# Optimization experiments

Hardware: AMD Instinct MI355X
Metric: run time of the kernel (lower is better)

Reference implementation:

```python
import jax, jax.numpy as jnp
import numpy as np

N_NODES = 50000
N_EDGES = 600000
D_IN = 128
HIDDEN = 128
N_REL = 8
N_LAYERS = 2


def setup_inputs() -> dict:
    key = jax.random.key(0)
    ks = jax.random.split(key, 10)
    node_feat = jax.random.normal(ks[0], (N_NODES, D_IN), dtype=jnp.float32)
    edge_index = jax.random.randint(ks[1], (2, N_EDGES), 0, N_NODES, dtype=jnp.int64)
    edge_type = jax.random.randint(ks[2], (N_EDGES,), 0, N_REL, dtype=jnp.int64)
    s = 1.0 / np.sqrt(D_IN)
    # stacked per-layer FastRGCNConv params (input_dim == hidden so shapes match)
    rel_w = jax.random.normal(ks[3], (N_LAYERS, N_REL, D_IN, HIDDEN), dtype=jnp.float32) * s
    root_w = jax.random.normal(ks[4], (N_LAYERS, D_IN, HIDDEN), dtype=jnp.float32) * s
    bias = jax.random.normal(ks[5], (N_LAYERS, HIDDEN), dtype=jnp.float32) * 0.01
    proj_w = jax.random.normal(ks[6], (N_LAYERS * HIDDEN, HIDDEN), dtype=jnp.float32) / np.sqrt(N_LAYERS * HIDDEN)
    proj_b = jax.random.normal(ks[7], (HIDDEN,), dtype=jnp.float32) * 0.01
    return {
        "node_feat": node_feat,
        "edge_index": edge_index,
        "edge_type": edge_type,
        "rel_w": rel_w,
        "root_w": root_w,
        "bias": bias,
        "proj_w": proj_w,
        "proj_b": proj_b,
    }


def _rgcn_layer(x, src, dst, etype, W, root, b):
    # FastRGCNConv: transform all nodes by all relations, then gather per edge.
    xW = jnp.einsum('nd,rdh->nrh', x, W)          # [N, R, H]
    m = xW[src, etype]                             # [E, H] per-edge message
    # mean aggregation per (target, relation), as in PyG FastRGCNConv aggr='mean'
    seg = dst * N_REL + etype                      # combined (target, relation) id
    cnt = jax.ops.segment_sum(jnp.ones_like(etype, dtype=x.dtype), seg,
                              num_segments=N_NODES * N_REL)
    norm = (1.0 / jnp.clip(cnt, 1.0, None))[seg]   # [E]
    agg = jax.ops.segment_sum(m * norm[:, None], dst, num_segments=N_NODES)
    return agg + x @ root + b


def reference(node_feat, edge_index, edge_type, rel_w, root_w, bias, proj_w, proj_b):
    src, dst = edge_index[0], edge_index[1]
    reps = []
    h = node_feat
    for i in range(N_LAYERS):
        h = _rgcn_layer(h, src, dst, edge_type, rel_w[i], root_w[i], bias[i])
        h = jax.nn.relu(h)
        reps.append(h)
    final = jnp.concatenate(reps, axis=-1) @ proj_w + proj_b
    return (final,) + tuple(reps)
```

## Files before the change

kernel.cpp:

```cpp
#include <hip/hip_runtime.h>
#include <hip/hip_bf16.h>

#define NN 50000
#define NE 600000
#define DD 128
#define RR 8
#define KY 1152

#define N2 (NN * RR)
#define SCHUNK 1024
#define NBS2 ((N2 + SCHUNK - 1) / SCHUNK)
#define MGRID ((NN + 127) / 128)

typedef __attribute__((ext_vector_type(8))) short short8;
typedef __attribute__((ext_vector_type(4))) float f32x4;
typedef __attribute__((ext_vector_type(4))) unsigned uint4v;

__device__ __forceinline__ unsigned short f2b(float x){
  __hip_bfloat16 h = __float2bfloat16(x);
  return __builtin_bit_cast(unsigned short, h);
}
__device__ __forceinline__ float blo(unsigned u){ return __builtin_bit_cast(float, u << 16); }
__device__ __forceinline__ float bhi(unsigned u){ return __builtin_bit_cast(float, u & 0xFFFF0000u); }
__device__ __forceinline__ unsigned pack2(float a, float b){
  return (unsigned)f2b(a) | ((unsigned)f2b(b) << 16);
}

#define GLDS16(g, l) __builtin_amdgcn_global_load_lds( \
    (const __attribute__((address_space(1))) void*)(g), \
    (__attribute__((address_space(3))) void*)(l), 16, 0, 0)

__global__ __launch_bounds__(256) void k_hist(const int* __restrict__ ei,
                                              const int* __restrict__ et,
                                              int* __restrict__ cnt) {
  int e = blockIdx.x * 256 + threadIdx.x;
  if (e < NE) {
    int dst = ei[NE + e];
    int r = et[e];
    atomicAdd(&cnt[dst * RR + r], 1);
  }
}

__global__ __launch_bounds__(256) void k_scan1(const int* __restrict__ cnt,
                                               int* __restrict__ bsum) {
  int b = blockIdx.x, t = threadIdx.x;
  int base = b * SCHUNK + t * 4;
  int s = 0;
  if (base < N2) {
    int4 v = *(const int4*)&cnt[base];
    s = v.x + v.y + v.z + v.w;
  }
  #pragma unroll
  for (int off = 32; off; off >>= 1) s += __shfl_down(s, off);
  __shared__ int wsum[4];
  int lane = t & 63, wv = t >> 6;
  if (lane == 0) wsum[wv] = s;
  __syncthreads();
  if (t == 0) bsum[b] = wsum[0] + wsum[1] + wsum[2] + wsum[3];
}

__global__ __launch_bounds__(512) void k_scan2(const int* __restrict__ bsum,
                                               int* __restrict__ boff) {
  int t = threadIdx.x, lane = t & 63, wv = t >> 6;
  int v = (t < NBS2) ? bsum[t] : 0;
  int x = v;
  #pragma unroll
  for (int off = 1; off < 64; off <<= 1) {
    int y = __shfl_up(x, off);
    if (lane >= off) x += y;
  }
  __shared__ int wt[8];
  if (lane == 63) wt[wv] = x;
  __syncthreads();
  int woff = 0;
  for (int w = 0; w < wv; w++) woff += wt[w];
  if (t < NBS2) boff[t] = woff + x - v;
}

__global__ __launch_bounds__(256) void k_scan3(const int* __restrict__ cnt,
                                               const int* __restrict__ boff,
                                               int* __restrict__ rp2,
                                               int* __restrict__ cur2) {
  int b = blockIdx.x, t = threadIdx.x;
  int lane = t & 63, wv = t >> 6;
  int base = b * SCHUNK + t * 4;
  int v[4] = {0, 0, 0, 0};
  int s = 0;
  if (base < N2) {
    int4 q = *(const int4*)&cnt[base];
    v[0] = q.x; v[1] = q.y; v[2] = q.z; v[3] = q.w;
    s = q.x + q.y + q.z + q.w;
  }
  int x = s;
  #pragma unroll
  for (int off = 1; off < 64; off <<= 1) {
    int y = __shfl_up(x, off);
    if (lane >= off) x += y;
  }
  __shared__ int wtot[4];
  if (lane == 63) wtot[wv] = x;
  __syncthreads();
  int woff = 0;
  for (int w = 0; w < wv; w++) woff += wtot[w];
  int exc = boff[b] + woff + x - s;
  if (base < N2) {
    #pragma unroll
    for (int j = 0; j < 4; j++) {
      cur2[base + j] = exc;
      rp2[base + j + 1] = exc + v[j];
      exc += v[j];
    }
  }
  if (b == 0 && t == 0) rp2[0] = 0;
}

__global__ __launch_bounds__(256) void k_scatter(const int* __restrict__ ei,
                                                 const int* __restrict__ et,
                                                 int* __restrict__ cur2,
                                                 unsigned* __restrict__ packed) {
  int e = blockIdx.x * 256 + threadIdx.x;
  if (e < NE) {
    int src = ei[e];
    int dst = ei[NE + e];
    int r = et[e];
    int p = atomicAdd(&cur2[dst * RR + r], 1);
    packed[p] = (unsigned)src | ((unsigned)r << 16);
  }
}

__global__ __launch_bounds__(256) void k_xb(const float* __restrict__ x,
                                            unsigned* __restrict__ xb2) {
  int i = blockIdx.x * 256 + threadIdx.x;
  if (i < NN * (DD / 2)) {
    float2 v = ((const float2*)x)[i];
    xb2[i] = pack2(v.x, v.y);
  }
}

__global__ __launch_bounds__(256) void k_wt2(const float* __restrict__ rel_w,
                                             const float* __restrict__ root_w,
                                             unsigned short* __restrict__ WT2) {
  int idx = blockIdx.x * 256 + threadIdx.x;
  if (idx >= 2 * KY * DD) return;
  int k = idx % DD;
  int j = (idx / DD) % KY;
  int l = idx / (DD * KY);
  float v;
  if (j < RR * DD) v = rel_w[(((size_t)l * RR + (j >> 7)) * DD + k) * DD + (j & 127)];
  else             v = root_w[((size_t)l * DD + k) * DD + (j - RR * DD)];
  WT2[idx] = f2b(v);
}

__global__ __launch_bounds__(256) void k_pt(const float* __restrict__ proj_w,
                                            unsigned short* __restrict__ PT) {
  int idx = blockIdx.x * 256 + threadIdx.x;
  if (idx >= DD * 256) return;
  int k = idx % 256;
  int n = idx / 256;
  PT[idx] = f2b(proj_w[(size_t)k * DD + n]);
}

__global__ __launch_bounds__(256) void k_ygemm(const unsigned short* __restrict__ A, int lda,
                                               const unsigned short* __restrict__ B2,
                                               unsigned short* __restrict__ Y) {
  __shared__ unsigned short smA[128 * 128];
  __shared__ unsigned short smB[128 * 128];
  int t = threadIdx.x;
  int rt = blockIdx.x % MGRID;
  int ct = blockIdx.x / MGRID;
  int lane = t & 63, wv = t >> 6;
  int wm = wv >> 1, wn = wv & 1;
  int l15 = lane & 15, lk = lane >> 4;

  #pragma unroll
  for (int i = 0; i < 8; i++) {
    int f = i * 256 + t;
    int row = f >> 4, cl = f & 15;
    int cg = cl ^ (row & 15);
    int rg = rt * 128 + row; if (rg >= NN) rg = NN - 1;
    GLDS16(A + (size_t)rg * lda + cg * 8, &smA[f * 8]);
  }
  #pragma unroll
  for (int i = 0; i < 8; i++) {
    int f = i * 256 + t;
    int row = f >> 4, cl = f & 15;
    int cg = cl ^ (row & 15);
    GLDS16(B2 + (size_t)(ct * 128 + row) * DD + cg * 8, &smB[f * 8]);
  }
  __syncthreads();

  f32x4 acc[4][4];
  #pragma unroll
  for (int mi = 0; mi < 4; mi++)
    #pragma unroll
    for (int ni = 0; ni < 4; ni++)
      acc[mi][ni] = (f32x4){0.f, 0.f, 0.f, 0.f};

  #pragma unroll
  for (int kk = 0; kk < 4; kk++) {
    short8 af[4], bf[4];
    #pragma unroll
    for (int q = 0; q < 4; q++) {
      int r  = wm * 64 + q * 16 + l15;
      int rb = wn * 64 + q * 16 + l15;
      int c  = kk * 4 + lk;
      af[q] = *(const short8*)&smA[r * 128 + ((c ^ (r & 15)) << 3)];
      bf[q] = *(const short8*)&smB[rb * 128 + ((c ^ (rb & 15)) << 3)];
    }
    #pragma unroll
    for (int mi = 0; mi < 4; mi++)
      #pragma unroll
      for (int ni = 0; ni < 4; ni++)
        acc[mi][ni] = __builtin_amdgcn_mfma_f32_16x16x32_bf16(af[mi], bf[ni], acc[mi][ni], 0, 0, 0);
  }
  __syncthreads();

  #pragma unroll
  for (int mi = 0; mi < 4; mi++)
    #pragma unroll
    for (int ni = 0; ni < 4; ni++) {
      int col = wn * 64 + ni * 16 + l15;
      #pragma unroll
      for (int j = 0; j < 4; j++) {
        int row = wm * 64 + mi * 16 + lk * 4 + j;
        smB[row * 128 + ((((col >> 3) ^ (row & 7)) << 3) | (col & 7))] = f2b(acc[mi][ni][j]);
      }
    }
  __syncthreads();

  {
    int row = t >> 1, half = t & 1;
    int rg = rt * 128 + row;
    if (rg < NN) {
      unsigned short* dst = Y + (size_t)rg * KY + ct * 128 + half * 64;
      #pragma unroll
      for (int i = 0; i < 8; i++) {
        int cc = half * 8 + i;
        ((uint4v*)dst)[i] = *(const uint4v*)&smB[row * 128 + ((cc ^ (row & 7)) << 3)];
      }
    }
  }
}

__global__ __launch_bounds__(256) void k_aggD(const unsigned short* __restrict__ Y,
                                              const unsigned* __restrict__ packed,
                                              const int* __restrict__ rp2,
                                              const float* __restrict__ bias,
                                              float* __restrict__ outf,
                                              unsigned short* __restrict__ hb, int hboff) {
  int v = blockIdx.x * 4 + (threadIdx.x >> 6);
  int lane = threadIdx.x & 63;
  int q = lane >> 4, sub = lane & 15;

  int f = 0;
  if (lane <= 8) f = rp2[v * RR + lane];
  int fn = __shfl(f, lane + 1);
  int c = fn - f;
  float winv = (lane < 8 && c > 0) ? 1.f / (float)c : 0.f;
  int e0 = __shfl(f, 0), e1 = __shfl(f, 8);

  float acc[8];
  #pragma unroll
  for (int j = 0; j < 8; j++) acc[j] = 0.f;

  for (int e = e0 + q; e < e1; e += 4) {
    unsigned rec = packed[e];
    int src = rec & 0xFFFF;
    int r = rec >> 16;
    float w = __shfl(winv, r);
    const uint4v* p = (const uint4v*)(Y + (size_t)src * KY + r * DD + sub * 8);
    uint4v u = *p;
    #pragma unroll
    for (int i = 0; i < 4; i++) {
      acc[2 * i]     += w * blo(u[i]);
      acc[2 * i + 1] += w * bhi(u[i]);
    }
  }

  if (q == 0) {
    uint4v u = *(const uint4v*)(Y + (size_t)v * KY + RR * DD + sub * 8);
    #pragma unroll
    for (int i = 0; i < 4; i++) {
      acc[2 * i]     += blo(u[i]);
      acc[2 * i + 1] += bhi(u[i]);
    }
  }

  #pragma unroll
  for (int j = 0; j < 8; j++) {
    acc[j] += __shfl_xor(acc[j], 32);
    acc[j] += __shfl_xor(acc[j], 16);
  }

  if (q == 0) {
    float4 b0 = *(const float4*)&bias[sub * 8];
    float4 b1 = *(const float4*)&bias[sub * 8 + 4];
    float val[8];
    val[0] = fmaxf(acc[0] + b0.x, 0.f); val[1] = fmaxf(acc[1] + b0.y, 0.f);
    val[2] = fmaxf(acc[2] + b0.z, 0.f); val[3] = fmaxf(acc[3] + b0.w, 0.f);
    val[4] = fmaxf(acc[4] + b1.x, 0.f); val[5] = fmaxf(acc[5] + b1.y, 0.f);
    val[6] = fmaxf(acc[6] + b1.z, 0.f); val[7] = fmaxf(acc[7] + b1.w, 0.f);
    float4* of = (float4*)&outf[(size_t)v * DD + sub * 8];
    of[0] = (float4){val[0], val[1], val[2], val[3]};
    of[1] = (float4){val[4], val[5], val[6], val[7]};
    uint4v hv;
    #pragma unroll
    for (int i = 0; i < 4; i++) hv[i] = pack2(val[2 * i], val[2 * i + 1]);
    *(uint4v*)(hb + (size_t)v * 256 + hboff + sub * 8) = hv;
  }
}

__global__ __launch_bounds__(256) void k_gemm(const unsigned short* __restrict__ A, int lda,
                                              const unsigned short* __restrict__ BT, int ldb,
                                              int M, int K,
                                              const float* __restrict__ bias,
                                              float* __restrict__ outf) {
  __shared__ unsigned short sA[128 * 64];
  __shared__ unsigned short sB[128 * 64];
  int t = threadIdx.x;
  int bm = blockIdx.x;
  int lane = t & 63, wv = t >> 6;
  int wm = wv >> 1, wn = wv & 1;
  int l15 = lane & 15, lk = lane >> 4;

  f32x4 acc[4][4];
  #pragma unroll
  for (int mi = 0; mi < 4; mi++)
    #pragma unroll
    for (int ni = 0; ni < 4; ni++)
      acc[mi][ni] = (f32x4){0.f, 0.f, 0.f, 0.f};

  int nkt = K >> 6;
  for (int kt = 0; kt < nkt; kt++) {
    #pragma unroll
    for (int i = 0; i < 4; i++) {
      int f = i * 256 + t;
      int row = f >> 3, cl = f & 7;
      int cg = cl ^ (row & 7);
      int rg = bm * 128 + row;
      if (rg >= M) rg = M - 1;
      GLDS16(A + (size_t)rg * lda + kt * 64 + cg * 8, &sA[f * 8]);
    }
    #pragma unroll
    for (int i = 0; i < 4; i++) {
      int f = i * 256 + t;
      int row = f >> 3, cl = f & 7;
      int cg = cl ^ (row & 7);
      GLDS16(BT + (size_t)row * ldb + kt * 64 + cg * 8, &sB[f * 8]);
    }
    __syncthreads();

    short8 af[4][2], bf[4][2];
    #pragma unroll
    for (int mi = 0; mi < 4; mi++) {
      #pragma unroll
      for (int kk = 0; kk < 2; kk++) {
        int r = wm * 64 + mi * 16 + l15;
        int c = kk * 4 + lk;
        af[mi][kk] = *(const short8*)&sA[((r << 3) + (c ^ (r & 7))) << 3];
        int rb = wn * 64 + mi * 16 + l15;
        bf[mi][kk] = *(const short8*)&sB[((rb << 3) + (c ^ (rb & 7))) << 3];
      }
    }
    #pragma unroll
    for (int mi = 0; mi < 4; mi++)
      #pragma unroll
      for (int ni = 0; ni < 4; ni++)
        #pragma unroll
        for (int kk = 0; kk < 2; kk++)
          acc[mi][ni] = __builtin_amdgcn_mfma_f32_16x16x32_bf16(af[mi][kk], bf[ni][kk], acc[mi][ni], 0, 0, 0);
    __syncthreads();
  }

  #pragma unroll
  for (int mi = 0; mi < 4; mi++) {
    #pragma unroll
    for (int ni = 0; ni < 4; ni++) {
      int cg = wn * 64 + ni * 16 + l15;
      float bv = bias[cg];
      #pragma unroll
      for (int j = 0; j < 4; j++) {
        int rg = bm * 128 + wm * 64 + mi * 16 + lk * 4 + j;
        if (rg < M) outf[(size_t)rg * 128 + cg] = acc[mi][ni][j] + bv;
      }
    }
  }
}

extern "C" void kernel_launch(void* const* d_in, const int* in_sizes, int n_in,
                              void* d_out, int out_size, void* d_ws, size_t ws_size,
                              hipStream_t stream) {
  const float* node_feat = (const float*)d_in[0];
  const int*   ei        = (const int*)d_in[1];
  const int*   et        = (const int*)d_in[2];
  const float* rel_w     = (const float*)d_in[3];
  const float* root_w    = (const float*)d_in[4];
  const float* bias      = (const float*)d_in[5];
  const float* proj_w    = (const float*)d_in[6];
  const float* proj_b    = (const float*)d_in[7];
  float* out = (float*)d_out;

  char* ws = (char*)d_ws;
  size_t off = 0;
  auto carve = [&](size_t bytes) { void* p = ws + off; off = (off + bytes + 255) & ~(size_t)255; return p; };
  unsigned short* Y    = (unsigned short*)carve((size_t)NN * KY * 2);
  unsigned short* Hb   = (unsigned short*)carve((size_t)NN * 256 * 2);
  unsigned short* xb   = (unsigned short*)carve((size_t)NN * DD * 2);
  unsigned short* WT2  = (unsigned short*)carve((size_t)2 * KY * DD * 2);
  unsigned short* PT   = (unsigned short*)carve((size_t)DD * 256 * 2);
  int* cnt_vr          = (int*)carve((size_t)N2 * 4);
  int* rp2             = (int*)carve((size_t)(N2 + 1) * 4);
  int* cur2            = (int*)carve((size_t)N2 * 4);
  unsigned* packed     = (unsigned*)carve((size_t)NE * 4);
  int* bsum            = (int*)carve((size_t)512 * 4);
  int* boff            = (int*)carve((size_t)512 * 4);
  (void)ws_size; (void)in_sizes; (void)n_in; (void)out_size;

  hipMemsetAsync(cnt_vr, 0, (size_t)N2 * 4, stream);

  int egrid = (NE + 255) / 256;
  k_hist<<<egrid, 256, 0, stream>>>(ei, et, cnt_vr);
  k_scan1<<<NBS2, 256, 0, stream>>>(cnt_vr, bsum);
  k_scan2<<<1, 512, 0, stream>>>(bsum, boff);
  k_scan3<<<NBS2, 256, 0, stream>>>(cnt_vr, boff, rp2, cur2);
  k_scatter<<<egrid, 256, 0, stream>>>(ei, et, cur2, packed);

  k_xb<<<(NN * (DD / 2) + 255) / 256, 256, 0, stream>>>(node_feat, (unsigned*)xb);
  k_wt2<<<(2 * KY * DD + 255) / 256, 256, 0, stream>>>(rel_w, root_w, WT2);
  k_pt<<<(DD * 256 + 255) / 256, 256, 0, stream>>>(proj_w, PT);

  k_ygemm<<<MGRID * 9, 256, 0, stream>>>(xb, DD, WT2, Y);
  k_aggD<<<NN / 4, 256, 0, stream>>>(Y, packed, rp2, bias,
                                     out + (size_t)NN * DD, Hb, 0);
  k_ygemm<<<MGRID * 9, 256, 0, stream>>>(Hb, 256, WT2 + (size_t)KY * DD, Y);
  k_aggD<<<NN / 4, 256, 0, stream>>>(Y, packed, rp2, bias + DD,
                                     out + (size_t)2 * NN * DD, Hb, DD);
  k_gemm<<<MGRID, 256, 0, stream>>>(Hb, 256, PT, 256, NN, 256, proj_b, out);
}
```

Baseline: 291.8 us.

## Load GEMM fragments directly from global memory with XCD-aware block remap

The Y-GEMM kernel no longer stages A and B tiles in shared memory. Each wave now loads its MFMA fragments straight from global memory, double-buffered in registers across the four k-steps. Block indices are also remapped so that consecutive tiles land on the same XCD, which should improve L2 reuse of the A rows shared across the 9 column tiles. This cuts LDS usage and removes one barrier, at the cost of more redundant global and L2 traffic, since each A fragment is now read by both wn waves.

```diff
diff --git a/kernel.cpp b/kernel.cpp
--- a/kernel.cpp
+++ b/kernel.cpp
@@ -163,31 +163,24 @@
 __global__ __launch_bounds__(256) void k_ygemm(const unsigned short* __restrict__ A, int lda,
                                                const unsigned short* __restrict__ B2,
                                                unsigned short* __restrict__ Y) {
-  __shared__ unsigned short smA[128 * 128];
-  __shared__ unsigned short smB[128 * 128];
+  __shared__ unsigned short smC[128 * 128];
   int t = threadIdx.x;
-  int rt = blockIdx.x % MGRID;
-  int ct = blockIdx.x / MGRID;
+  const int nb = MGRID * 9, q8 = nb >> 3, r8 = nb & 7;
+  int xcd = blockIdx.x & 7, idx = blockIdx.x >> 3;
+  int w = (xcd < r8 ? xcd * (q8 + 1) : r8 * (q8 + 1) + (xcd - r8) * q8) + idx;
+  int rt = w / 9, ct = w % 9;
+
   int lane = t & 63, wv = t >> 6;
   int wm = wv >> 1, wn = wv & 1;
   int l15 = lane & 15, lk = lane >> 4;
 
-  #pragma unroll
-  for (int i = 0; i < 8; i++) {
-    int f = i * 256 + t;
-    int row = f >> 4, cl = f & 15;
-    int cg = cl ^ (row & 15);
-    int rg = rt * 128 + row; if (rg >= NN) rg = NN - 1;
-    GLDS16(A + (size_t)rg * lda + cg * 8, &smA[f * 8]);
-  }
-  #pragma unroll
-  for (int i = 0; i < 8; i++) {
-    int f = i * 256 + t;
-    int row = f >> 4, cl = f & 15;
-    int cg = cl ^ (row & 15);
-    GLDS16(B2 + (size_t)(ct * 128 + row) * DD + cg * 8, &smB[f * 8]);
-  }
-  __syncthreads();
+  size_t aoff[4], boff4[4];
+  #pragma unroll
+  for (int q = 0; q < 4; q++) {
+    int rg = rt * 128 + wm * 64 + q * 16 + l15; if (rg >= NN) rg = NN - 1;
+    aoff[q] = (size_t)rg * lda;
+    boff4[q] = (size_t)(ct * 128 + wn * 64 + q * 16 + l15) * DD;
+  }
 
   f32x4 acc[4][4];
   #pragma unroll
@@ -196,24 +189,42 @@
     for (int ni = 0; ni < 4; ni++)
       acc[mi][ni] = (f32x4){0.f, 0.f, 0.f, 0.f};
 
+  short8 afA[4], bfA[4], afB[4], bfB[4];
+  #pragma unroll
+  for (int q = 0; q < 4; q++) {
+    afA[q] = *(const short8*)(A + aoff[q] + lk * 8);
+    bfA[q] = *(const short8*)(B2 + boff4[q] + lk * 8);
+  }
   #pragma unroll
   for (int kk = 0; kk < 4; kk++) {
-    short8 af[4], bf[4];
-    #pragma unroll
-    for (int q = 0; q < 4; q++) {
-      int r  = wm * 64 + q * 16 + l15;
-      int rb = wn * 64 + q * 16 + l15;
-      int c  = kk * 4 + lk;
-      af[q] = *(const short8*)&smA[r * 128 + ((c ^ (r & 15)) << 3)];
-      bf[q] = *(const short8*)&smB[rb * 128 + ((c ^ (rb & 15)) << 3)];
-    }
-    #pragma unroll
-    for (int mi = 0; mi < 4; mi++)
-      #pragma unroll
-      for (int ni = 0; ni < 4; ni++)
-        acc[mi][ni] = __builtin_amdgcn_mfma_f32_16x16x32_bf16(af[mi], bf[ni], acc[mi][ni], 0, 0, 0);
-  }
-  __syncthreads();
+    if ((kk & 1) == 0) {
+      if (kk < 3) {
+        #pragma unroll
+        for (int q = 0; q < 4; q++) {
+          afB[q] = *(const short8*)(A + aoff[q] + ((kk + 1) * 4 + lk) * 8);
+          bfB[q] = *(const short8*)(B2 + boff4[q] + ((kk + 1) * 4 + lk) * 8);
+        }
+      }
+      #pragma unroll
+      for (int mi = 0; mi < 4; mi++)
+        #pragma unroll
+        for (int ni = 0; ni < 4; ni++)
+          acc[mi][ni] = __builtin_amdgcn_mfma_f32_16x16x32_bf16(afA[mi], bfA[ni], acc[mi][ni], 0, 0, 0);
+    } else {
+      if (kk < 3) {
+        #pragma unroll
+        for (int q = 0; q < 4; q++) {
+          afA[q] = *(const short8*)(A + aoff[q] + ((kk + 1) * 4 + lk) * 8);
+          bfA[q] = *(const short8*)(B2 + boff4[q] + ((kk + 1) * 4 + lk) * 8);
+        }
+      }
+      #pragma unroll
+      for (int mi = 0; mi < 4; mi++)
+        #pragma unroll
+        for (int ni = 0; ni < 4; ni++)
+          acc[mi][ni] = __builtin_amdgcn_mfma_f32_16x16x32_bf16(afB[mi], bfB[ni], acc[mi][ni], 0, 0, 0);
+    }
+  }
 
   #pragma unroll
   for (int mi = 0; mi < 4; mi++)
@@ -223,7 +234,7 @@
       #pragma unroll
       for (int j = 0; j < 4; j++) {
         int row = wm * 64 + mi * 16 + lk * 4 + j;
-        smB[row * 128 + ((((col >> 3) ^ (row & 7)) << 3) | (col & 7))] = f2b(acc[mi][ni][j]);
+        smC[row * 128 + ((((col >> 3) ^ (row & 7)) << 3) | (col & 7))] = f2b(acc[mi][ni][j]);
       }
     }
   __syncthreads();
@@ -236,7 +247,7 @@
       #pragma unroll
       for (int i = 0; i < 8; i++) {
         int cc = half * 8 + i;
-        ((uint4v*)dst)[i] = *(const uint4v*)&smB[row * 128 + ((cc ^ (row & 7)) << 3)];
+        ((uint4v*)dst)[i] = *(const uint4v*)&smC[row * 128 + ((cc ^ (row & 7)) << 3)];
       }
     }
   }
```

Result: slower. 338.6 us (+16.1%).
